# Kernel tuning notes

Measured on AMD Instinct MI355X. Metric: run time of the kernel, lower is better.

Reference implementation:

```python
import jax, jax.numpy as jnp
import numpy as np
import math

B, S_MAX, D = 16, 4096, 4096
H, H_KV, D_H = 32, 8, 128
REP = H // H_KV
START_POS = S_MAX - 1  # decode at last slot -> attend over full cache


def _rope(t, cos, sin):
    # t: [B, 1, h, D_H]; cos/sin: [1, D_H//2] (per-position rotary factors)
    b, s, h, dh = t.shape
    tr = t.reshape(b, s, h, dh // 2, 2)
    e, o = tr[..., 0], tr[..., 1]          # even / odd components
    c = cos[None, :, None, :]              # [1, 1, 1, D_H//2]
    sn = sin[None, :, None, :]
    out = jnp.stack([e * c - o * sn, e * sn + o * c], axis=-1)
    return out.reshape(b, s, h, dh)


def setup_inputs() -> dict:
    key = jax.random.key(0)
    ks = jax.random.split(key, 8)
    x = jax.random.normal(ks[0], (B, 1, D), dtype=jnp.float32)
    cache_k = jax.random.normal(ks[1], (B, S_MAX, H_KV, D_H), dtype=jnp.float32) * 0.02
    cache_v = jax.random.normal(ks[2], (B, S_MAX, H_KV, D_H), dtype=jnp.float32) * 0.02
    wq = jax.random.normal(ks[3], (D, H * D_H), dtype=jnp.float32) * 0.02
    wk = jax.random.normal(ks[4], (D, H_KV * D_H), dtype=jnp.float32) * 0.02
    wv = jax.random.normal(ks[5], (D, H_KV * D_H), dtype=jnp.float32) * 0.02
    wo = jax.random.normal(ks[6], (H * D_H, D), dtype=jnp.float32) * 0.02
    # real RoPE angles for position START_POS
    inv_freq = 1.0 / (10000.0 ** (np.arange(0, D_H, 2, dtype=np.float32) / D_H))
    ang = np.float32(START_POS) * inv_freq  # [D_H//2]
    freqs_cos = jnp.asarray(np.cos(ang))[None, :]  # [1, 64]
    freqs_sin = jnp.asarray(np.sin(ang))[None, :]
    return {"x": x, "cache_k": cache_k, "cache_v": cache_v,
            "wq": wq, "wk": wk, "wv": wv, "wo": wo,
            "freqs_cos": freqs_cos, "freqs_sin": freqs_sin,
            "start_pos": START_POS}


def reference(x, cache_k, cache_v, wq, wk, wv, wo, freqs_cos, freqs_sin, start_pos):
    b = x.shape[0]
    xq = (x @ wq).reshape(b, 1, H, D_H)
    xk = (x @ wk).reshape(b, 1, H_KV, D_H)
    xv = (x @ wv).reshape(b, 1, H_KV, D_H)
    xq = _rope(xq, freqs_cos, freqs_sin)
    xk = _rope(xk, freqs_cos, freqs_sin)
    # KV-cache append (start_pos is a Python int -> static slice)
    cache_k = jax.lax.dynamic_update_slice(cache_k, xk, (0, start_pos, 0, 0))
    cache_v = jax.lax.dynamic_update_slice(cache_v, xv, (0, start_pos, 0, 0))
    L = start_pos + 1
    keys = cache_k[:, :L]    # [B, L, H_KV, D_H]
    # NOTE: original has `values = repeat_kv(keys, num_rep)` -- values == keys (bug),
    # reproduced faithfully here. cache_v is still written, matching the original.
    q = xq.reshape(b, 1, H_KV, REP, D_H)
    # GQA scores without materializing the repeated KV tensor
    scores = jnp.einsum('bqkrd,bskd->bkrqs', q, keys) / math.sqrt(D_H)
    attn = jax.nn.softmax(scores, axis=-1)
    out = jnp.einsum('bkrqs,bskd->bqkrd', attn, keys)  # values == keys (faithful bug)
    out = out.reshape(b, 1, H * D_H) @ wo
    return out
```

## Files before the change

kernel.cpp:

```cpp
#include <hip/hip_runtime.h>
#include <math.h>

#define BATCH 16
#define SMAX 4096
#define DMODEL 4096
#define NH 32
#define NKV 8
#define NREP 4
#define DH 128
#define QKCOLS 5120
#define NCHUNK 8
#define CHUNK 512
#define TILE 64
#define NCH 64
#define GD 64

__global__ __launch_bounds__(256) void gemv_part(
    const float* __restrict__ in,
    const float* __restrict__ w1, int c1,
    const float* __restrict__ w2, int c2,
    float* __restrict__ part)
{
    const int t = threadIdx.x;
    const int col = blockIdx.x * 512 + t * 2;
    const int totC = c1 + c2;
    const int d0 = blockIdx.y * GD;

    const float* w; int stride, wc;
    if (col < c1) { w = w1; stride = c1; wc = col; }
    else          { w = w2; stride = c2; wc = col - c1; }
    const float* wp = w + (size_t)d0 * stride + wc;

    float2 acc[BATCH];
#pragma unroll
    for (int b = 0; b < BATCH; ++b) acc[b] = make_float2(0.f, 0.f);

#pragma unroll 4
    for (int i = 0; i < GD; ++i) {
        const float2 wv = *(const float2*)(wp + (size_t)i * stride);
#pragma unroll
        for (int b = 0; b < BATCH; ++b) {
            const float xv = in[(size_t)b * DMODEL + d0 + i];
            acc[b].x = fmaf(wv.x, xv, acc[b].x);
            acc[b].y = fmaf(wv.y, xv, acc[b].y);
        }
    }
    const size_t base = (size_t)blockIdx.y * BATCH;
#pragma unroll
    for (int b = 0; b < BATCH; ++b)
        *(float2*)&part[(base + b) * totC + col] = acc[b];
}

__global__ __launch_bounds__(256) void rope_reduce(
    const float* __restrict__ part,
    const float* __restrict__ fcos, const float* __restrict__ fsin,
    float* __restrict__ xqk)
{
    int g = blockIdx.x * 256 + threadIdx.x;
    int b = g / 2560;
    int po = g % 2560;
    float e = 0.f, o = 0.f;
    const float* p = part + (size_t)b * QKCOLS + 2 * po;
#pragma unroll 8
    for (int ch = 0; ch < NCH; ++ch) {
        float2 v = *(const float2*)(p + (size_t)ch * BATCH * QKCOLS);
        e += v.x; o += v.y;
    }
    int i = po & 63;
    float c = fcos[i], s = fsin[i];
    xqk[(size_t)b * QKCOLS + 2 * po]     = e * c - o * s;
    xqk[(size_t)b * QKCOLS + 2 * po + 1] = e * s + o * c;
}

__global__ __launch_bounds__(256, 4) void attn_part_kernel(
    const float* __restrict__ cache_k,
    const float* __restrict__ xqk,
    const int* __restrict__ sp,
    float* __restrict__ out)
{
    const int chunk = blockIdx.x;
    const int kv = blockIdx.y;
    const int b = blockIdx.z;
    const int t = threadIdx.x;
    const int dl = t & 63;
    const int r = t >> 6;
    const int start_pos = sp[0];

    __shared__ float k_lds[TILE * DH];
    __shared__ float q_lds[NREP * DH];
    __shared__ float p_lds[NREP * TILE];

    const float* xknew = xqk + (size_t)b * QKCOLS + DMODEL + kv * DH;
    const float* kbase = cache_k + ((size_t)b * SMAX * NKV + kv) * DH;
    const float scale = 0.08838834764831845f;

    {
        const float* qp0 = xqk + (size_t)b * QKCOLS + (kv * NREP) * DH;
        q_lds[t]       = qp0[t] * scale;
        q_lds[256 + t] = qp0[256 + t] * scale;
    }

    float4 st[8];

#define STAGE(TT) do {                                                        \
        const int s_b_ = chunk * CHUNK + (TT) * TILE;                         \
        _Pragma("unroll")                                                     \
        for (int it = 0; it < 8; ++it) {                                      \
            int f_ = it * 256 + t;                                            \
            int row_ = f_ >> 5;                                               \
            int c4_ = f_ & 31;                                                \
            int s_ = s_b_ + row_;                                             \
            const float* src_ = (s_ == start_pos) ? (xknew + 4 * c4_)         \
                              : (kbase + (size_t)s_ * (NKV * DH) + 4 * c4_);  \
            st[it] = *(const float4*)src_;                                    \
        }                                                                     \
    } while (0)

#define KWRITE() do {                                                         \
        _Pragma("unroll")                                                     \
        for (int it = 0; it < 8; ++it) {                                      \
            int f_ = it * 256 + t;                                            \
            int row_ = f_ >> 5;                                               \
            int c4_ = f_ & 31;                                                \
            *(float4*)&k_lds[row_ * DH + ((c4_ ^ (row_ & 7)) << 2)] = st[it]; \
        }                                                                     \
    } while (0)

    STAGE(0);
    KWRITE();
    __syncthreads();

    float m_run = -1e30f, l_run = 0.f;
    float ax = 0.f, ay = 0.f;
    const float* qh = q_lds + r * DH;
    const float* krow = k_lds + dl * DH;
    const int sw = dl & 7;
    const int c4o = dl >> 1;
    const int o2 = (2 * dl) & 3;

    for (int tt = 0; tt < CHUNK / TILE; ++tt) {
        if (tt < CHUNK / TILE - 1) STAGE(tt + 1);

        const int s_base = chunk * CHUNK + tt * TILE;

        float c0 = 0.f, c1 = 0.f, c2 = 0.f, c3 = 0.f;
#pragma unroll 4
        for (int i = 0; i < 32; ++i) {
            const float4 q4 = *(const float4*)(qh + 4 * i);
            const float4 k4 = *(const float4*)(krow + ((i ^ sw) << 2));
            c0 = fmaf(q4.x, k4.x, c0);
            c1 = fmaf(q4.y, k4.y, c1);
            c2 = fmaf(q4.z, k4.z, c2);
            c3 = fmaf(q4.w, k4.w, c3);
        }
        float score = (c0 + c1) + (c2 + c3);
        if (s_base + dl > start_pos) score = -1e30f;

        float m_tile = score;
#pragma unroll
        for (int m = 1; m < 64; m <<= 1)
            m_tile = fmaxf(m_tile, __shfl_xor(m_tile, m, 64));
        float m_new = fmaxf(m_run, m_tile);
        float alpha = __expf(m_run - m_new);
        float p = __expf(score - m_new);
        float psum = p;
#pragma unroll
        for (int m = 1; m < 64; m <<= 1)
            psum += __shfl_xor(psum, m, 64);
        l_run = l_run * alpha + psum;
        ax *= alpha; ay *= alpha;
        m_run = m_new;

        p_lds[r * TILE + dl] = p;
        __syncthreads();

#pragma unroll 4
        for (int j4 = 0; j4 < 16; ++j4) {
            const float4 pj = *(const float4*)&p_lds[r * TILE + 4 * j4];
#define PVROW(JJ, PV) do {                                                    \
            const int rw_ = 4 * j4 + (JJ);                                    \
            const float2 k2_ = *(const float2*)&k_lds[rw_ * DH +              \
                                   ((c4o ^ (rw_ & 7)) << 2) + o2];            \
            ax = fmaf((PV), k2_.x, ax);                                       \
            ay = fmaf((PV), k2_.y, ay);                                       \
        } while (0)
            PVROW(0, pj.x);
            PVROW(1, pj.y);
            PVROW(2, pj.z);
            PVROW(3, pj.w);
#undef PVROW
        }
        __syncthreads();

        if (tt < CHUNK / TILE - 1) {
            KWRITE();
            __syncthreads();
        }
    }

    float* rec = out + ((((size_t)b * NKV + kv) * NCHUNK + chunk) * NREP + r) * 130;
    rec[2 * dl] = ax;
    rec[2 * dl + 1] = ay;
    if (dl == 0) { rec[128] = m_run; rec[129] = l_run; }
#undef STAGE
#undef KWRITE
}

__global__ __launch_bounds__(128) void attn_combine(
    const float* __restrict__ part, float* __restrict__ attn_out)
{
    const int hq = blockIdx.x;
    const int b = blockIdx.y;
    const int kv = hq >> 2, r = hq & 3;
    const int d = threadIdx.x;
    float m_c[NCHUNK], l_c[NCHUNK];
    float M = -1e30f;
#pragma unroll
    for (int c = 0; c < NCHUNK; ++c) {
        const float* rec = part + ((((size_t)b * NKV + kv) * NCHUNK + c) * NREP + r) * 130;
        m_c[c] = rec[128]; l_c[c] = rec[129];
        M = fmaxf(M, m_c[c]);
    }
    float num = 0.f, den = 0.f;
#pragma unroll
    for (int c = 0; c < NCHUNK; ++c) {
        const float* rec = part + ((((size_t)b * NKV + kv) * NCHUNK + c) * NREP + r) * 130;
        float w = __expf(m_c[c] - M);
        num = fmaf(w, rec[d], num);
        den = fmaf(w, l_c[c], den);
    }
    attn_out[(size_t)b * DMODEL + hq * DH + d] = num / den;
}

__global__ __launch_bounds__(256) void reduce_out(
    const float* __restrict__ part, float* __restrict__ out)
{
    int g = blockIdx.x * 256 + threadIdx.x;
    int b = g >> 12, o = g & 4095;
    float s = 0.f;
#pragma unroll 8
    for (int ch = 0; ch < NCH; ++ch)
        s += part[((size_t)ch * BATCH + b) * DMODEL + o];
    out[g] = s;
}

extern "C" void kernel_launch(void* const* d_in, const int* in_sizes, int n_in,
                              void* d_out, int out_size, void* d_ws, size_t ws_size,
                              hipStream_t stream) {
    const float* x       = (const float*)d_in[0];
    const float* cache_k = (const float*)d_in[1];
    const float* wq      = (const float*)d_in[3];
    const float* wk      = (const float*)d_in[4];
    const float* wo      = (const float*)d_in[6];
    const float* fcos    = (const float*)d_in[7];
    const float* fsin    = (const float*)d_in[8];
    const int*   sp      = (const int*)d_in[9];
    float* out = (float*)d_out;
    float* ws  = (float*)d_ws;

    float* part_qk   = ws;
    float* xqk       = part_qk + 5242880;
    float* attn_part = xqk + 81920;
    float* attn_out  = attn_part + 532480;
    float* part_out  = part_qk;

    gemv_part<<<dim3(QKCOLS / 512, NCH), 256, 0, stream>>>(x, wq, 4096, wk, 1024, part_qk);
    rope_reduce<<<160, 256, 0, stream>>>(part_qk, fcos, fsin, xqk);
    attn_part_kernel<<<dim3(NCHUNK, NKV, BATCH), 256, 0, stream>>>(cache_k, xqk, sp, attn_part);
    attn_combine<<<dim3(NH, BATCH), 128, 0, stream>>>(attn_part, attn_out);
    gemv_part<<<dim3(DMODEL / 512, NCH), 256, 0, stream>>>(attn_out, wo, 4096, nullptr, 0, part_out);
    reduce_out<<<256, 256, 0, stream>>>(part_out, out);
}
```

Measured before the change: 628.5 us.

## Split QK dot across warps with register-held queries and LDS partial reduction

The attention partial kernel now has each wavefront own a 32-wide slice of the head dimension, with all four query heads' slices held in registers. Each K row read from LDS is reused across the four heads, and partial scores are reduced through a new shared buffer. The PV accumulation is remapped so each lane handles a head/column pair, and the rescale factor is broadcast via LDS. This cuts redundant LDS reads of K at the cost of an extra barrier per tile and more registers. The GEMV unroll is also raised from 4 to 8.

```diff
diff --git a/kernel.cpp b/kernel.cpp
--- a/kernel.cpp
+++ b/kernel.cpp
@@ -35,7 +35,7 @@
 #pragma unroll
     for (int b = 0; b < BATCH; ++b) acc[b] = make_float2(0.f, 0.f);
 
-#pragma unroll 4
+#pragma unroll 8
     for (int i = 0; i < GD; ++i) {
         const float2 wv = *(const float2*)(wp + (size_t)i * stride);
 #pragma unroll
@@ -83,12 +83,14 @@
     const int b = blockIdx.z;
     const int t = threadIdx.x;
     const int dl = t & 63;
-    const int r = t >> 6;
+    const int w = t >> 6;
     const int start_pos = sp[0];
 
     __shared__ float k_lds[TILE * DH];
     __shared__ float q_lds[NREP * DH];
+    __shared__ float sp_lds[NREP * NREP * TILE];
     __shared__ float p_lds[NREP * TILE];
+    __shared__ float a_lds[NREP];
 
     const float* xknew = xqk + (size_t)b * QKCOLS + DMODEL + kv * DH;
     const float* kbase = cache_k + ((size_t)b * SMAX * NKV + kv) * DH;
@@ -130,30 +132,53 @@
     KWRITE();
     __syncthreads();
 
+    float4 q4r[NREP][8];
+#pragma unroll
+    for (int r = 0; r < NREP; ++r)
+#pragma unroll
+        for (int i = 0; i < 8; ++i)
+            q4r[r][i] = *(const float4*)&q_lds[r * DH + w * 32 + 4 * i];
+
+    const int sw = dl & 7;
+    const int rp = dl >> 4;
+    const int pair = dl & 15;
+    const int c4p = w * 8 + (pair >> 1);
+    const int o2p = 2 * (pair & 1);
+
     float m_run = -1e30f, l_run = 0.f;
     float ax = 0.f, ay = 0.f;
-    const float* qh = q_lds + r * DH;
-    const float* krow = k_lds + dl * DH;
-    const int sw = dl & 7;
-    const int c4o = dl >> 1;
-    const int o2 = (2 * dl) & 3;
 
     for (int tt = 0; tt < CHUNK / TILE; ++tt) {
         if (tt < CHUNK / TILE - 1) STAGE(tt + 1);
 
         const int s_base = chunk * CHUNK + tt * TILE;
 
-        float c0 = 0.f, c1 = 0.f, c2 = 0.f, c3 = 0.f;
-#pragma unroll 4
-        for (int i = 0; i < 32; ++i) {
-            const float4 q4 = *(const float4*)(qh + 4 * i);
-            const float4 k4 = *(const float4*)(krow + ((i ^ sw) << 2));
-            c0 = fmaf(q4.x, k4.x, c0);
-            c1 = fmaf(q4.y, k4.y, c1);
-            c2 = fmaf(q4.z, k4.z, c2);
-            c3 = fmaf(q4.w, k4.w, c3);
+        float4 kr[8];
+#pragma unroll
+        for (int i = 0; i < 8; ++i)
+            kr[i] = *(const float4*)&k_lds[dl * DH + ((w * 8 + (i ^ sw)) << 2)];
+        float pr0 = 0.f, pr1 = 0.f, pr2 = 0.f, pr3 = 0.f;
+#pragma unroll
+        for (int i = 0; i < 8; ++i) {
+            pr0 = fmaf(q4r[0][i].x, kr[i].x, pr0); pr0 = fmaf(q4r[0][i].y, kr[i].y, pr0);
+            pr0 = fmaf(q4r[0][i].z, kr[i].z, pr0); pr0 = fmaf(q4r[0][i].w, kr[i].w, pr0);
+            pr1 = fmaf(q4r[1][i].x, kr[i].x, pr1); pr1 = fmaf(q4r[1][i].y, kr[i].y, pr1);
+            pr1 = fmaf(q4r[1][i].z, kr[i].z, pr1); pr1 = fmaf(q4r[1][i].w, kr[i].w, pr1);
+            pr2 = fmaf(q4r[2][i].x, kr[i].x, pr2); pr2 = fmaf(q4r[2][i].y, kr[i].y, pr2);
+            pr2 = fmaf(q4r[2][i].z, kr[i].z, pr2); pr2 = fmaf(q4r[2][i].w, kr[i].w, pr2);
+            pr3 = fmaf(q4r[3][i].x, kr[i].x, pr3); pr3 = fmaf(q4r[3][i].y, kr[i].y, pr3);
+            pr3 = fmaf(q4r[3][i].z, kr[i].z, pr3); pr3 = fmaf(q4r[3][i].w, kr[i].w, pr3);
         }
-        float score = (c0 + c1) + (c2 + c3);
+        sp_lds[(w * NREP + 0) * TILE + dl] = pr0;
+        sp_lds[(w * NREP + 1) * TILE + dl] = pr1;
+        sp_lds[(w * NREP + 2) * TILE + dl] = pr2;
+        sp_lds[(w * NREP + 3) * TILE + dl] = pr3;
+        __syncthreads();
+
+        float score = sp_lds[(0 * NREP + w) * TILE + dl]
+                    + sp_lds[(1 * NREP + w) * TILE + dl]
+                    + sp_lds[(2 * NREP + w) * TILE + dl]
+                    + sp_lds[(3 * NREP + w) * TILE + dl];
         if (s_base + dl > start_pos) score = -1e30f;
 
         float m_tile = score;
@@ -168,19 +193,21 @@
         for (int m = 1; m < 64; m <<= 1)
             psum += __shfl_xor(psum, m, 64);
         l_run = l_run * alpha + psum;
-        ax *= alpha; ay *= alpha;
         m_run = m_new;
 
-        p_lds[r * TILE + dl] = p;
+        p_lds[w * TILE + dl] = p;
+        if (dl == 0) a_lds[w] = alpha;
         __syncthreads();
 
-#pragma unroll 4
+        const float al = a_lds[rp];
+        ax *= al; ay *= al;
+#pragma unroll
         for (int j4 = 0; j4 < 16; ++j4) {
-            const float4 pj = *(const float4*)&p_lds[r * TILE + 4 * j4];
+            const float4 pj = *(const float4*)&p_lds[rp * TILE + 4 * j4];
 #define PVROW(JJ, PV) do {                                                    \
             const int rw_ = 4 * j4 + (JJ);                                    \
             const float2 k2_ = *(const float2*)&k_lds[rw_ * DH +              \
-                                   ((c4o ^ (rw_ & 7)) << 2) + o2];            \
+                                   ((c4p ^ (rw_ & 7)) << 2) + o2p];           \
             ax = fmaf((PV), k2_.x, ax);                                       \
             ay = fmaf((PV), k2_.y, ay);                                       \
         } while (0)
@@ -192,16 +219,16 @@
         }
         __syncthreads();
 
-        if (tt < CHUNK / TILE - 1) {
-            KWRITE();
-            __syncthreads();
-        }
-    }
-
-    float* rec = out + ((((size_t)b * NKV + kv) * NCHUNK + chunk) * NREP + r) * 130;
-    rec[2 * dl] = ax;
-    rec[2 * dl + 1] = ay;
-    if (dl == 0) { rec[128] = m_run; rec[129] = l_run; }
+        if (tt < CHUNK / TILE - 1) KWRITE();
+        __syncthreads();
+    }
+
+    float* rec = out + ((((size_t)b * NKV + kv) * NCHUNK + chunk) * NREP + rp) * 130;
+    *(float2*)&rec[w * 32 + 2 * pair] = make_float2(ax, ay);
+    if (dl == 0) {
+        float* recw = out + ((((size_t)b * NKV + kv) * NCHUNK + chunk) * NREP + w) * 130;
+        recw[128] = m_run; recw[129] = l_run;
+    }
 #undef STAGE
 #undef KWRITE
 }
```

Measured after the change: 803.7 us. +27.9%, slower.
